# Kernel optimization log

Hardware: AMD Instinct MI355X
Metric: run time of the kernel (lower is better)

## Reference

```python
import jax, jax.numpy as jnp
import numpy as np

B, C, L = 128, 1, 4096


def setup_inputs() -> dict:
    key = jax.random.key(0)
    x_0 = jax.random.normal(key, (B, C, L), dtype=jnp.float32)
    return {"x_0": x_0}


def reference(x_0):
    # Original: per-sample F.conv1d(x, flip(x), padding=L-1).
    # Cross-correlation with a flipped kernel == full linear convolution:
    #   out[b, t] = sum_c sum_i x[b,c,i] * x[b,c,t-i],  t in [0, 2L-2]
    # Vectorized over batch and channels via vmap; summed over channels
    # (conv1d contracts input channels against the weight's channel dim).
    conv = jax.vmap(jax.vmap(lambda a: jnp.convolve(a, a, mode='full')))(x_0)  # [B, C, 2L-1]
    return conv.sum(axis=1)[:, None, :]  # [B, 1, 2L-1]
```

## Files before the change

kernel.cpp:

```cpp
#include <hip/hip_runtime.h>

#define LL     4096
#define OUTL   8191
#define FPAD   272
#define NPAIRF 2340
#define CSTRF  2952
#define REVB   11808
#define BTOP   5895
#define NG     968
#define LDS_DW 15680

typedef short v8s __attribute__((ext_vector_type(8)));
typedef float v4f __attribute__((ext_vector_type(4)));

__device__ __forceinline__ unsigned bf16b(float f) {
    unsigned u = __builtin_bit_cast(unsigned, f);
    u += 0x7fff + ((u >> 16) & 1);
    return u >> 16;
}
__device__ __forceinline__ int physdw(int r, int p) { return r * CSTRF + p + 2 * (p >> 3); }
__device__ __forceinline__ int revdw(int g) { return REVB + 4 * (g ^ ((g >> 3) & 7)); }

struct Frag { uint2 a0l, a0h, a1l, a1h; uint4 b0, b1, b2, b3; };

__global__ __launch_bounds__(256)
void selfconv_mfma3(const float* __restrict__ xg, float* __restrict__ outg) {
    __shared__ unsigned lds[LDS_DW];
    const int tid = threadIdx.x;
    const int blk = blockIdx.x;
    const int h2 = blk >> 8;
    const int b  = (blk & 255) >> 1;
    const int rg = (blk & 1) + 2 * h2;
    const int T0 = rg << 11;
    const float* __restrict__ xb = xg + b * LL;

    for (int r = 0; r < 4; ++r)
        for (int pp = tid; pp < NPAIRF / 2; pp += 256) {
            int p = 2 * pp;
            int e = 4 * pp + r - FPAD;
            float f0 = (e >= 0 && e < LL) ? xb[e] : 0.f;
            float f1 = (e + 1 >= 0 && e + 1 < LL) ? xb[e + 1] : 0.f;
            float f2 = (e + 2 >= 0 && e + 2 < LL) ? xb[e + 2] : 0.f;
            float f3 = (e + 3 >= 0 && e + 3 < LL) ? xb[e + 3] : 0.f;
            uint2 w;
            w.x = bf16b(f0) | (bf16b(f1) << 16);
            w.y = bf16b(f2) | (bf16b(f3) << 16);
            *(uint2*)&lds[physdw(r, p)] = w;
        }
    for (int g = tid; g < NG; g += 256) {
        unsigned w[4];
#pragma unroll
        for (int d = 0; d < 4; ++d) {
            int xlo = BTOP - (8 * g + 2 * d);
            int xhi = xlo - 1;
            float flo = (xlo >= 0 && xlo < LL) ? xb[xlo] : 0.f;
            float fhi = (xhi >= 0 && xhi < LL) ? xb[xhi] : 0.f;
            w[d] = bf16b(flo) | (bf16b(fhi) << 16);
        }
        *(uint4*)&lds[revdw(g)] = uint4{w[0], w[1], w[2], w[3]};
    }
    __syncthreads();

    const int wv   = tid >> 6;
    const int lane = tid & 63;
    const int ln16 = lane & 15;
    const int q    = lane >> 4;

    int mn = 0x7fffffff, mx = -0x7fffffff;
#pragma unroll
    for (int u = 0; u < 2; ++u)
#pragma unroll
        for (int v = 0; v < 4; ++v) {
            int base = T0 + 256 * u + 512 * v;
            int iLo = base - (LL - 1); if (iLo < 0) iLo = 0;
            int iHi = base + 255;      if (iHi > LL - 1) iHi = LL - 1;
            int a = iLo - 256 * u; if (a < mn) mn = a;
            int c2 = iHi - 256 * u; if (c2 > mx) mx = c2;
        }
    const int base_   = mn - 15;
    const int i0start = base_ - ((base_ - 1) & 7);
    const int nch     = ((mx - i0start) >> 5) + 1;
    const int nw      = (nch - wv + 3) >> 2;
    const int cmax    = nw - 1;
    const int i0w     = i0start + 32 * wv;

    int uA = i0w + ln16 + 8 * q + FPAD;
    int rA = uA & 3, pA = (uA >> 2) << 1;
    const int awA0 = physdw(rA, pA), awA1 = physdw(rA, pA + 2);
    const int gB0 = ((BTOP - T0 + i0w) >> 3) - 2 * ln16 + q;

    v4f acc00{0,0,0,0}, acc01{0,0,0,0}, acc02{0,0,0,0}, acc03{0,0,0,0};
    v4f acc10{0,0,0,0}, acc11{0,0,0,0}, acc12{0,0,0,0}, acc13{0,0,0,0};

    auto ld = [&](Frag& F, int c) {
        int ic = c > cmax ? cmax : c;
        int oA = 80 * ic;
        F.a0l = *(const uint2*)&lds[awA0 + oA];
        F.a0h = *(const uint2*)&lds[awA1 + oA];
        F.a1l = *(const uint2*)&lds[awA0 + oA + 160];
        F.a1h = *(const uint2*)&lds[awA1 + oA + 160];
        int g = gB0 + 16 * ic;
        F.b0 = *(const uint4*)&lds[revdw(g)];
        F.b1 = *(const uint4*)&lds[revdw(g - 64)];
        F.b2 = *(const uint4*)&lds[revdw(g - 128)];
        F.b3 = *(const uint4*)&lds[revdw(g - 192)];
    };
    auto mk2 = [](uint2 lo, uint2 hi) {
        union { unsigned u[4]; v8s s; } z;
        z.u[0] = lo.x; z.u[1] = lo.y; z.u[2] = hi.x; z.u[3] = hi.y; return z.s;
    };
    auto mk4 = [](uint4 v) {
        union { unsigned u[4]; v8s s; } z;
        z.u[0] = v.x; z.u[1] = v.y; z.u[2] = v.z; z.u[3] = v.w; return z.s;
    };
    auto cmp = [&](const Frag& F) {
        v8s A0 = mk2(F.a0l, F.a0h), A1 = mk2(F.a1l, F.a1h);
        v8s B0 = mk4(F.b0), B1 = mk4(F.b1), B2 = mk4(F.b2), B3 = mk4(F.b3);
        acc00 = __builtin_amdgcn_mfma_f32_16x16x32_bf16(A0, B0, acc00, 0, 0, 0);
        acc10 = __builtin_amdgcn_mfma_f32_16x16x32_bf16(A1, B0, acc10, 0, 0, 0);
        acc01 = __builtin_amdgcn_mfma_f32_16x16x32_bf16(A0, B1, acc01, 0, 0, 0);
        acc11 = __builtin_amdgcn_mfma_f32_16x16x32_bf16(A1, B1, acc11, 0, 0, 0);
        acc02 = __builtin_amdgcn_mfma_f32_16x16x32_bf16(A0, B2, acc02, 0, 0, 0);
        acc12 = __builtin_amdgcn_mfma_f32_16x16x32_bf16(A1, B2, acc12, 0, 0, 0);
        acc03 = __builtin_amdgcn_mfma_f32_16x16x32_bf16(A0, B3, acc03, 0, 0, 0);
        acc13 = __builtin_amdgcn_mfma_f32_16x16x32_bf16(A1, B3, acc13, 0, 0, 0);
    };

    Frag F0, F1, F2;
    ld(F0, 0); ld(F1, 1);
    int c = 0;
    for (; c + 3 <= nw; c += 3) {
        ld(F2, c + 2); cmp(F0);
        ld(F0, c + 3); cmp(F1);
        ld(F1, c + 4); cmp(F2);
    }
    if (c < nw)     cmp(F0);
    if (c + 1 < nw) cmp(F1);

    __syncthreads();
    float* fs = (float*)lds;
    if (wv > 0) {
        int sb = ((wv - 1) * 64 + lane) * 36;
        *(v4f*)&fs[sb]      = acc00; *(v4f*)&fs[sb + 4]  = acc10;
        *(v4f*)&fs[sb + 8]  = acc01; *(v4f*)&fs[sb + 12] = acc11;
        *(v4f*)&fs[sb + 16] = acc02; *(v4f*)&fs[sb + 20] = acc12;
        *(v4f*)&fs[sb + 24] = acc03; *(v4f*)&fs[sb + 28] = acc13;
    }
    __syncthreads();
    if (wv == 0) {
#pragma unroll
        for (int s = 0; s < 3; ++s) {
            int sb = (s * 64 + lane) * 36;
            acc00 += *(const v4f*)&fs[sb];      acc10 += *(const v4f*)&fs[sb + 4];
            acc01 += *(const v4f*)&fs[sb + 8];  acc11 += *(const v4f*)&fs[sb + 12];
            acc02 += *(const v4f*)&fs[sb + 16]; acc12 += *(const v4f*)&fs[sb + 20];
            acc03 += *(const v4f*)&fs[sb + 24]; acc13 += *(const v4f*)&fs[sb + 28];
        }
        float* __restrict__ ob = outg + b * OUTL;
        const v4f* accs[8] = {&acc00, &acc10, &acc01, &acc11,
                              &acc02, &acc12, &acc03, &acc13};
#pragma unroll
        for (int uv = 0; uv < 8; ++uv) {
            int u = uv & 1, v = uv >> 1;
            int tb = T0 + 256 * u + 512 * v + 4 * q + 16 * ln16;
            v4f a = *accs[uv];
#pragma unroll
            for (int r2 = 0; r2 < 4; ++r2)
                if (tb + r2 < OUTL) ob[tb + r2] = a[r2];
        }
    }
}

extern "C" void kernel_launch(void* const* d_in, const int* in_sizes, int n_in,
                              void* d_out, int out_size, void* d_ws, size_t ws_size,
                              hipStream_t stream) {
    const float* x = (const float*)d_in[0];
    float* out = (float*)d_out;
    selfconv_mfma3<<<dim3(512), dim3(256), 0, stream>>>(x, out);
}
```

Before: 74.21 us.

## Use 8-wave blocks with two-phase LDS layout and tree reduction

Doubles the block to 512 threads (8 waves), so each wave handles half as many K-chunks. The A operand moves from four phase-shifted bf16 copies to two (even/odd) with scalar dword loads, which shrinks LDS so more blocks fit per CU. The B swizzle is simplified, and the tile order is permuted so heavy and light output regions interleave across blocks. The cross-wave reduction becomes two stages, which adds barriers, and the scalar A loads raise LDS instruction count.

```diff
diff --git a/kernel.cpp b/kernel.cpp
--- a/kernel.cpp
+++ b/kernel.cpp
@@ -1,14 +1,14 @@
 #include <hip/hip_runtime.h>
 
-#define LL     4096
-#define OUTL   8191
-#define FPAD   272
-#define NPAIRF 2340
-#define CSTRF  2952
-#define REVB   11808
-#define BTOP   5895
-#define NG     968
-#define LDS_DW 15680
+#define LL    4096
+#define OUTL  8191
+#define FPAD  272
+#define NPDW  2336
+#define CB1   2352
+#define RB    4704
+#define BTOP  5887
+#define NGU   971
+#define LDSDW 9472
 
 typedef short v8s __attribute__((ext_vector_type(8)));
 typedef float v4f __attribute__((ext_vector_type(4)));
@@ -18,53 +18,44 @@
     u += 0x7fff + ((u >> 16) & 1);
     return u >> 16;
 }
-__device__ __forceinline__ int physdw(int r, int p) { return r * CSTRF + p + 2 * (p >> 3); }
-__device__ __forceinline__ int revdw(int g) { return REVB + 4 * (g ^ ((g >> 3) & 7)); }
 
-struct Frag { uint2 a0l, a0h, a1l, a1h; uint4 b0, b1, b2, b3; };
+struct Frag { unsigned a[4], a2[4]; uint4 b3, b2, b1, b0; };
 
-__global__ __launch_bounds__(256)
-void selfconv_mfma3(const float* __restrict__ xg, float* __restrict__ outg) {
-    __shared__ unsigned lds[LDS_DW];
+__global__ __launch_bounds__(512, 4)
+void selfconv_mfma5(const float* __restrict__ xg, float* __restrict__ outg) {
+    __shared__ unsigned lds[LDSDW];
     const int tid = threadIdx.x;
     const int blk = blockIdx.x;
-    const int h2 = blk >> 8;
-    const int b  = (blk & 255) >> 1;
-    const int rg = (blk & 1) + 2 * h2;
-    const int T0 = rg << 11;
+    const int b   = blk & 127;
+    const int id  = blk >> 7;
+    const int rg  = (id == 0) ? 0 : (id == 1) ? 3 : (id == 2) ? 1 : 2;
+    const int T0  = rg << 11;
     const float* __restrict__ xb = xg + b * LL;
 
-    for (int r = 0; r < 4; ++r)
-        for (int pp = tid; pp < NPAIRF / 2; pp += 256) {
-            int p = 2 * pp;
-            int e = 4 * pp + r - FPAD;
-            float f0 = (e >= 0 && e < LL) ? xb[e] : 0.f;
-            float f1 = (e + 1 >= 0 && e + 1 < LL) ? xb[e + 1] : 0.f;
-            float f2 = (e + 2 >= 0 && e + 2 < LL) ? xb[e + 2] : 0.f;
-            float f3 = (e + 3 >= 0 && e + 3 < LL) ? xb[e + 3] : 0.f;
-            uint2 w;
-            w.x = bf16b(f0) | (bf16b(f1) << 16);
-            w.y = bf16b(f2) | (bf16b(f3) << 16);
-            *(uint2*)&lds[physdw(r, p)] = w;
-        }
-    for (int g = tid; g < NG; g += 256) {
+    for (int idx = tid; idx < 2 * NPDW; idx += 512) {
+        int r = idx >= NPDW ? 1 : 0;
+        int p = idx - r * NPDW;
+        int e = 2 * p + r - FPAD;
+        float f0 = (e >= 0 && e < LL) ? xb[e] : 0.f;
+        float f1 = (e + 1 >= 0 && e + 1 < LL) ? xb[e + 1] : 0.f;
+        lds[(r ? CB1 : 0) + p] = bf16b(f0) | (bf16b(f1) << 16);
+    }
+    for (int g = tid; g < NGU; g += 512) {
         unsigned w[4];
 #pragma unroll
         for (int d = 0; d < 4; ++d) {
-            int xlo = BTOP - (8 * g + 2 * d);
+            int xlo = BTOP - 8 * g - 2 * d;
             int xhi = xlo - 1;
             float flo = (xlo >= 0 && xlo < LL) ? xb[xlo] : 0.f;
             float fhi = (xhi >= 0 && xhi < LL) ? xb[xhi] : 0.f;
             w[d] = bf16b(flo) | (bf16b(fhi) << 16);
         }
-        *(uint4*)&lds[revdw(g)] = uint4{w[0], w[1], w[2], w[3]};
+        int P = g ^ ((g >> 4) & 1);
+        *(uint4*)&lds[RB + 4 * P] = uint4{w[0], w[1], w[2], w[3]};
     }
     __syncthreads();
 
-    const int wv   = tid >> 6;
-    const int lane = tid & 63;
-    const int ln16 = lane & 15;
-    const int q    = lane >> 4;
+    const int wv = tid >> 6, lane = tid & 63, ln16 = lane & 15, q = lane >> 4;
 
     int mn = 0x7fffffff, mx = -0x7fffffff;
 #pragma unroll
@@ -80,85 +71,97 @@
     const int base_   = mn - 15;
     const int i0start = base_ - ((base_ - 1) & 7);
     const int nch     = ((mx - i0start) >> 5) + 1;
-    const int nw      = (nch - wv + 3) >> 2;
-    const int cmax    = nw - 1;
+    const int nw      = (nch - wv + 7) >> 3;
     const int i0w     = i0start + 32 * wv;
 
-    int uA = i0w + ln16 + 8 * q + FPAD;
-    int rA = uA & 3, pA = (uA >> 2) << 1;
-    const int awA0 = physdw(rA, pA), awA1 = physdw(rA, pA + 2);
-    const int gB0 = ((BTOP - T0 + i0w) >> 3) - 2 * ln16 + q;
+    const int s0p = i0w + ln16 + 8 * q + FPAD;
+    int aw = (s0p >> 1) + ((s0p & 1) ? CB1 : 0);
+    const int g3 = (BTOP - T0 - 1536 - 16 * ln16 + i0w + 8 * q) >> 3;
+    int bw = RB + 4 * (g3 ^ ((g3 >> 4) & 1));
 
-    v4f acc00{0,0,0,0}, acc01{0,0,0,0}, acc02{0,0,0,0}, acc03{0,0,0,0};
-    v4f acc10{0,0,0,0}, acc11{0,0,0,0}, acc12{0,0,0,0}, acc13{0,0,0,0};
+    v4f a00{0,0,0,0}, a01{0,0,0,0}, a02{0,0,0,0}, a03{0,0,0,0};
+    v4f a10{0,0,0,0}, a11{0,0,0,0}, a12{0,0,0,0}, a13{0,0,0,0};
 
-    auto ld = [&](Frag& F, int c) {
-        int ic = c > cmax ? cmax : c;
-        int oA = 80 * ic;
-        F.a0l = *(const uint2*)&lds[awA0 + oA];
-        F.a0h = *(const uint2*)&lds[awA1 + oA];
-        F.a1l = *(const uint2*)&lds[awA0 + oA + 160];
-        F.a1h = *(const uint2*)&lds[awA1 + oA + 160];
-        int g = gB0 + 16 * ic;
-        F.b0 = *(const uint4*)&lds[revdw(g)];
-        F.b1 = *(const uint4*)&lds[revdw(g - 64)];
-        F.b2 = *(const uint4*)&lds[revdw(g - 128)];
-        F.b3 = *(const uint4*)&lds[revdw(g - 192)];
+    auto ld = [&](Frag& F, int a, int w) {
+        F.a[0]  = lds[a];       F.a[1]  = lds[a + 1];
+        F.a[2]  = lds[a + 2];   F.a[3]  = lds[a + 3];
+        F.a2[0] = lds[a + 128]; F.a2[1] = lds[a + 129];
+        F.a2[2] = lds[a + 130]; F.a2[3] = lds[a + 131];
+        F.b3 = *(const uint4*)&lds[w];
+        F.b2 = *(const uint4*)&lds[w + 256];
+        F.b1 = *(const uint4*)&lds[w + 512];
+        F.b0 = *(const uint4*)&lds[w + 768];
     };
-    auto mk2 = [](uint2 lo, uint2 hi) {
-        union { unsigned u[4]; v8s s; } z;
-        z.u[0] = lo.x; z.u[1] = lo.y; z.u[2] = hi.x; z.u[3] = hi.y; return z.s;
+    auto mkA = [](const unsigned (&u)[4]) {
+        union { unsigned x[4]; v8s s; } z;
+        z.x[0] = u[0]; z.x[1] = u[1]; z.x[2] = u[2]; z.x[3] = u[3]; return z.s;
     };
-    auto mk4 = [](uint4 v) {
-        union { unsigned u[4]; v8s s; } z;
-        z.u[0] = v.x; z.u[1] = v.y; z.u[2] = v.z; z.u[3] = v.w; return z.s;
+    auto mkB = [](uint4 v) {
+        union { unsigned x[4]; v8s s; } z;
+        z.x[0] = v.x; z.x[1] = v.y; z.x[2] = v.z; z.x[3] = v.w; return z.s;
     };
     auto cmp = [&](const Frag& F) {
-        v8s A0 = mk2(F.a0l, F.a0h), A1 = mk2(F.a1l, F.a1h);
-        v8s B0 = mk4(F.b0), B1 = mk4(F.b1), B2 = mk4(F.b2), B3 = mk4(F.b3);
-        acc00 = __builtin_amdgcn_mfma_f32_16x16x32_bf16(A0, B0, acc00, 0, 0, 0);
-        acc10 = __builtin_amdgcn_mfma_f32_16x16x32_bf16(A1, B0, acc10, 0, 0, 0);
-        acc01 = __builtin_amdgcn_mfma_f32_16x16x32_bf16(A0, B1, acc01, 0, 0, 0);
-        acc11 = __builtin_amdgcn_mfma_f32_16x16x32_bf16(A1, B1, acc11, 0, 0, 0);
-        acc02 = __builtin_amdgcn_mfma_f32_16x16x32_bf16(A0, B2, acc02, 0, 0, 0);
-        acc12 = __builtin_amdgcn_mfma_f32_16x16x32_bf16(A1, B2, acc12, 0, 0, 0);
-        acc03 = __builtin_amdgcn_mfma_f32_16x16x32_bf16(A0, B3, acc03, 0, 0, 0);
-        acc13 = __builtin_amdgcn_mfma_f32_16x16x32_bf16(A1, B3, acc13, 0, 0, 0);
+        v8s A0 = mkA(F.a), A1 = mkA(F.a2);
+        v8s B0 = mkB(F.b0), B1 = mkB(F.b1), B2 = mkB(F.b2), B3 = mkB(F.b3);
+        a00 = __builtin_amdgcn_mfma_f32_16x16x32_bf16(A0, B0, a00, 0, 0, 0);
+        a10 = __builtin_amdgcn_mfma_f32_16x16x32_bf16(A1, B0, a10, 0, 0, 0);
+        a01 = __builtin_amdgcn_mfma_f32_16x16x32_bf16(A0, B1, a01, 0, 0, 0);
+        a11 = __builtin_amdgcn_mfma_f32_16x16x32_bf16(A1, B1, a11, 0, 0, 0);
+        a02 = __builtin_amdgcn_mfma_f32_16x16x32_bf16(A0, B2, a02, 0, 0, 0);
+        a12 = __builtin_amdgcn_mfma_f32_16x16x32_bf16(A1, B2, a12, 0, 0, 0);
+        a03 = __builtin_amdgcn_mfma_f32_16x16x32_bf16(A0, B3, a03, 0, 0, 0);
+        a13 = __builtin_amdgcn_mfma_f32_16x16x32_bf16(A1, B3, a13, 0, 0, 0);
     };
 
-    Frag F0, F1, F2;
-    ld(F0, 0); ld(F1, 1);
+    Frag F0, F1;
+    int awE = aw, bwE = bw, awO = aw + 128, bwO = bw + 128;
+    ld(F0, awE, bwE); awE += 256; bwE += 256;
+    ld(F1, awO, bwO); awO += 256; bwO += 256;
     int c = 0;
-    for (; c + 3 <= nw; c += 3) {
-        ld(F2, c + 2); cmp(F0);
-        ld(F0, c + 3); cmp(F1);
-        ld(F1, c + 4); cmp(F2);
+    for (; c + 2 < nw; c += 2) {
+        cmp(F0); ld(F0, awE, bwE); awE += 256; bwE += 256;
+        cmp(F1); ld(F1, awO, bwO); awO += 256; bwO += 256;
     }
-    if (c < nw)     cmp(F0);
+    cmp(F0);
     if (c + 1 < nw) cmp(F1);
 
+    float* fs = (float*)lds;
     __syncthreads();
-    float* fs = (float*)lds;
-    if (wv > 0) {
-        int sb = ((wv - 1) * 64 + lane) * 36;
-        *(v4f*)&fs[sb]      = acc00; *(v4f*)&fs[sb + 4]  = acc10;
-        *(v4f*)&fs[sb + 8]  = acc01; *(v4f*)&fs[sb + 12] = acc11;
-        *(v4f*)&fs[sb + 16] = acc02; *(v4f*)&fs[sb + 20] = acc12;
-        *(v4f*)&fs[sb + 24] = acc03; *(v4f*)&fs[sb + 28] = acc13;
+    if (wv >= 4) {
+        int sb = (wv - 4) * 2304 + lane * 36;
+        *(v4f*)&fs[sb]      = a00; *(v4f*)&fs[sb + 4]  = a10;
+        *(v4f*)&fs[sb + 8]  = a01; *(v4f*)&fs[sb + 12] = a11;
+        *(v4f*)&fs[sb + 16] = a02; *(v4f*)&fs[sb + 20] = a12;
+        *(v4f*)&fs[sb + 24] = a03; *(v4f*)&fs[sb + 28] = a13;
+    }
+    __syncthreads();
+    if (wv < 4) {
+        int sb = wv * 2304 + lane * 36;
+        a00 += *(const v4f*)&fs[sb];      a10 += *(const v4f*)&fs[sb + 4];
+        a01 += *(const v4f*)&fs[sb + 8];  a11 += *(const v4f*)&fs[sb + 12];
+        a02 += *(const v4f*)&fs[sb + 16]; a12 += *(const v4f*)&fs[sb + 20];
+        a03 += *(const v4f*)&fs[sb + 24]; a13 += *(const v4f*)&fs[sb + 28];
+    }
+    __syncthreads();
+    if (wv >= 1 && wv < 4) {
+        int sb = (wv - 1) * 2304 + lane * 36;
+        *(v4f*)&fs[sb]      = a00; *(v4f*)&fs[sb + 4]  = a10;
+        *(v4f*)&fs[sb + 8]  = a01; *(v4f*)&fs[sb + 12] = a11;
+        *(v4f*)&fs[sb + 16] = a02; *(v4f*)&fs[sb + 20] = a12;
+        *(v4f*)&fs[sb + 24] = a03; *(v4f*)&fs[sb + 28] = a13;
     }
     __syncthreads();
     if (wv == 0) {
 #pragma unroll
         for (int s = 0; s < 3; ++s) {
-            int sb = (s * 64 + lane) * 36;
-            acc00 += *(const v4f*)&fs[sb];      acc10 += *(const v4f*)&fs[sb + 4];
-            acc01 += *(const v4f*)&fs[sb + 8];  acc11 += *(const v4f*)&fs[sb + 12];
-            acc02 += *(const v4f*)&fs[sb + 16]; acc12 += *(const v4f*)&fs[sb + 20];
-            acc03 += *(const v4f*)&fs[sb + 24]; acc13 += *(const v4f*)&fs[sb + 28];
+            int sb = s * 2304 + lane * 36;
+            a00 += *(const v4f*)&fs[sb];      a10 += *(const v4f*)&fs[sb + 4];
+            a01 += *(const v4f*)&fs[sb + 8];  a11 += *(const v4f*)&fs[sb + 12];
+            a02 += *(const v4f*)&fs[sb + 16]; a12 += *(const v4f*)&fs[sb + 20];
+            a03 += *(const v4f*)&fs[sb + 24]; a13 += *(const v4f*)&fs[sb + 28];
         }
         float* __restrict__ ob = outg + b * OUTL;
-        const v4f* accs[8] = {&acc00, &acc10, &acc01, &acc11,
-                              &acc02, &acc12, &acc03, &acc13};
+        const v4f* accs[8] = {&a00, &a10, &a01, &a11, &a02, &a12, &a03, &a13};
 #pragma unroll
         for (int uv = 0; uv < 8; ++uv) {
             int u = uv & 1, v = uv >> 1;
@@ -176,5 +179,5 @@
                               hipStream_t stream) {
     const float* x = (const float*)d_in[0];
     float* out = (float*)d_out;
-    selfconv_mfma3<<<dim3(512), dim3(256), 0, stream>>>(x, out);
+    selfconv_mfma5<<<dim3(512), dim3(512), 0, stream>>>(x, out);
 }
```

Measured after the change: 65.21 us. -12.1%, faster.
